# Optimization experiments

Hardware: AMD Instinct MI355X
Metric: run time of the kernel (lower is better)

## Reference

```python
import jax, jax.numpy as jnp
import numpy as np

D_MODEL = 1024
NUM_HEADS = 16
HEAD_DIM = D_MODEL // NUM_HEADS
MAX_SEQ_LEN = 2048
THETA = 10000.0
B, T = 2, 2048


def precompute_cos_sin(head_dim, max_len, theta):
    freqs = 1.0 / theta ** (jnp.arange(0, head_dim, 2, dtype=jnp.float32) / head_dim)
    t = jnp.arange(max_len, dtype=jnp.float32)
    f = jnp.outer(t, freqs)  # [max_len, head_dim//2]
    return jnp.concatenate([jnp.cos(f), jnp.sin(f)], axis=-1)  # [max_len, head_dim]


def apply_rotary_emb(x, cos_sin):
    # x: [B, H, T, Hs]; cos_sin: [T, Hs]
    xr = x.reshape(*x.shape[:-1], -1, 2)
    x1, x2 = xr[..., 0], xr[..., 1]
    cos, sin = jnp.split(cos_sin, 2, axis=-1)  # each [T, Hs//2]
    out = jnp.stack([x1 * cos - x2 * sin, x1 * sin + x2 * cos], axis=-1)
    return out.reshape(x.shape).astype(x.dtype)


def setup_inputs() -> dict:
    key = jax.random.key(0)
    ks = jax.random.split(key, 5)
    scale = 1.0 / np.sqrt(D_MODEL)
    return {
        'x': jax.random.normal(ks[0], (B, T, D_MODEL), dtype=jnp.float32),
        'wq': jax.random.normal(ks[1], (D_MODEL, D_MODEL), dtype=jnp.float32) * scale,
        'wk': jax.random.normal(ks[2], (D_MODEL, D_MODEL), dtype=jnp.float32) * scale,
        'wv': jax.random.normal(ks[3], (D_MODEL, D_MODEL), dtype=jnp.float32) * scale,
        'wo': jax.random.normal(ks[4], (D_MODEL, D_MODEL), dtype=jnp.float32) * scale,
    }


def reference(x, wq, wk, wv, wo):
    seq_len = x.shape[1]
    # Linear: einsum('...i,oi->...o'), weight stored as [out, in]
    q = jnp.einsum('bti,oi->bto', x, wq)
    k = jnp.einsum('bti,oi->bto', x, wk)
    v = jnp.einsum('bti,oi->bto', x, wv)
    # split heads: B T (nH Hs) -> B nH T Hs
    def split_heads(t):
        return t.reshape(t.shape[0], t.shape[1], NUM_HEADS, HEAD_DIM).transpose(0, 2, 1, 3)
    xq, xk, xv = split_heads(q), split_heads(k), split_heads(v)
    cos_sin = precompute_cos_sin(HEAD_DIM, MAX_SEQ_LEN, THETA)[:seq_len]
    xq = apply_rotary_emb(xq, cos_sin)
    xk = apply_rotary_emb(xk, cos_sin)
    scores = jnp.einsum('bhqd,bhkd->bhqk', xq, xk) / jnp.sqrt(jnp.float32(HEAD_DIM))
    causal = jnp.tril(jnp.ones((seq_len, seq_len), dtype=bool))
    scores = jnp.where(causal[None, None], scores, -jnp.inf)
    attn = jax.nn.softmax(scores, axis=-1)
    xo = jnp.einsum('bhqk,bhkd->bhqd', attn, xv)
    xo = xo.transpose(0, 2, 1, 3).reshape(x.shape[0], seq_len, D_MODEL)
    return jnp.einsum('bti,oi->bto', xo, wo)
```

## Files before the change

kernel.cpp:

```cpp
#include <hip/hip_runtime.h>
#include <hip/hip_bf16.h>

typedef __hip_bfloat16 bf16;
using s8v = __attribute__((ext_vector_type(8))) short;
using s4v = __attribute__((ext_vector_type(4))) short;
using f4v = __attribute__((ext_vector_type(4))) float;

#define D_MODEL 1024
#define NHEADS  16
#define HDIM    64
#define TSEQ    2048
#define NBATCH  2
#define BT      (NBATCH * TSEQ)

#define QSCALE  0.180336880111f
#define SBIAS  -17.3123404907f

__device__ inline short f2bf_bits(float f) {
    bf16 h = __float2bfloat16(f);
    return *reinterpret_cast<short*>(&h);
}

__device__ inline void load8(const bf16* p, s8v& o) { o = *(const s8v*)p; }
__device__ inline void load8(const float* p, s8v& o) {
    const f4v a = *(const f4v*)p;
    const f4v b = *(const f4v*)(p + 4);
    s8v r;
    r[0] = f2bf_bits(a[0]); r[1] = f2bf_bits(a[1]);
    r[2] = f2bf_bits(a[2]); r[3] = f2bf_bits(a[3]);
    r[4] = f2bf_bits(b[0]); r[5] = f2bf_bits(b[1]);
    r[6] = f2bf_bits(b[2]); r[7] = f2bf_bits(b[3]);
    o = r;
}

__device__ inline void storeC(bf16* p, float v)  { *p = __float2bfloat16(v); }
__device__ inline void storeC(float* p, float v) { *p = v; }

__device__ inline void gload_lds16(const bf16* g, short* l) {
    __builtin_amdgcn_global_load_lds(
        (__attribute__((address_space(1))) void*)(unsigned long long)(size_t)g,
        (__attribute__((address_space(3))) void*)l,
        16, 0, 0);
}

__device__ inline void stage8(const bf16* g, short* l) { gload_lds16(g, l); }
__device__ inline void stage8(const float* g, short* l) {
    s8v v; load8(g, v); *(s8v*)l = v;
}

__global__ __launch_bounds__(256) void cvt_kernel(
    const float* __restrict__ src, bf16* __restrict__ dst)
{
    const size_t i = ((size_t)blockIdx.x * 256 + threadIdx.x) * 8;
    s8v v; load8(src + i, v);
    *(s8v*)&dst[i] = v;
}

__global__ __launch_bounds__(256) void cvt_all_kernel(
    const float* __restrict__ x,  bf16* __restrict__ xb,
    const float* __restrict__ wq, bf16* __restrict__ wqb,
    const float* __restrict__ wk, bf16* __restrict__ wkb,
    const float* __restrict__ wv, bf16* __restrict__ wvb,
    const float* __restrict__ wo, bf16* __restrict__ wob,
    float2* __restrict__ cs_table)
{
    const int blk = blockIdx.x;
    if (blk >= 4096) {
        const int idx = (blk - 4096) * 256 + threadIdx.x;
        const int tt = idx >> 5;
        const int i  = idx & 31;
        const float inv_freq = expf(-(float)i * (9.210340371976184f / 32.0f));
        float s, c;
        sincosf((float)tt * inv_freq, &s, &c);
        cs_table[idx] = make_float2(c, s);
        return;
    }
    const float* src; bf16* dst; int base;
    if (blk < 2048)      { src = x;  dst = xb;  base = 0; }
    else if (blk < 2560) { src = wq; dst = wqb; base = 2048; }
    else if (blk < 3072) { src = wk; dst = wkb; base = 2560; }
    else if (blk < 3584) { src = wv; dst = wvb; base = 3072; }
    else                 { src = wo; dst = wob; base = 3584; }
    const size_t i = ((size_t)(blk - base) * 256 + threadIdx.x) * 8;
    s8v v; load8(src + i, v);
    *(s8v*)&dst[i] = v;
}

template <int TM, bool ROPE, typename TA, typename TW, typename TC>
__global__ __launch_bounds__(256, 2) void gemm_bt(
    const TA* __restrict__ A,
    const TW* __restrict__ W0, const TW* __restrict__ W1, const TW* __restrict__ W2,
    TC* __restrict__ C0, TC* __restrict__ C1, TC* __restrict__ C2,
    bf16* __restrict__ VT, const float2* __restrict__ cs_table)
{
    const TW* W = (blockIdx.z == 0) ? W0 : (blockIdx.z == 1) ? W1 : W2;
    TC*       C = (blockIdx.z == 0) ? C0 : (blockIdx.z == 1) ? C1 : C2;
    const bool vt_mode = (VT != nullptr) && (blockIdx.z == 2);

    constexpr int K = 1024, N = 1024;
    constexpr int MT = TM / 32;
    __shared__ __align__(16) short As[TM * 64];
    __shared__ __align__(16) short Ws[128 * 64];

    const int t    = threadIdx.x;
    const int lane = t & 63;
    const int wave = t >> 6;
    const int m16  = lane & 15;
    const int quad = lane >> 4;
    const int wm   = (wave >> 1) * (TM / 2);
    const int wn   = (wave & 1) * 64;
    const int rowBase = blockIdx.x * TM;
    const int colBase = blockIdx.y * 128;

    f4v acc[MT][4];
#pragma unroll
    for (int i = 0; i < MT; ++i)
#pragma unroll
        for (int j = 0; j < 4; ++j) acc[i][j] = f4v{0.f, 0.f, 0.f, 0.f};

    for (int kk = 0; kk < K / 64; ++kk) {
#pragma unroll
        for (int r = 0; r < TM / 32; ++r) {
            const int chunk = r * 256 + t;
            const int row   = chunk >> 3;
            const int c8s   = (chunk & 7) ^ (row & 7);
            stage8(A + (size_t)(rowBase + row) * K + kk * 64 + c8s * 8, &As[chunk * 8]);
        }
#pragma unroll
        for (int r = 0; r < 4; ++r) {
            const int chunk = r * 256 + t;
            const int row   = chunk >> 3;
            const int c8s   = (chunk & 7) ^ (row & 7);
            stage8(W + (size_t)(colBase + row) * K + kk * 64 + c8s * 8, &Ws[chunk * 8]);
        }
        __syncthreads();

#pragma unroll
        for (int ks = 0; ks < 2; ++ks) {
            s8v af[MT], bw[4];
#pragma unroll
            for (int mt = 0; mt < MT; ++mt) {
                const int rowa = wm + mt * 16 + m16;
                af[mt] = *(const s8v*)&As[rowa * 64 + ((ks * 4 + quad) ^ (rowa & 7)) * 8];
            }
#pragma unroll
            for (int nt = 0; nt < 4; ++nt) {
                const int roww = wn + nt * 16 + m16;
                bw[nt] = *(const s8v*)&Ws[roww * 64 + ((ks * 4 + quad) ^ (roww & 7)) * 8];
            }
#pragma unroll
            for (int mt = 0; mt < MT; ++mt)
#pragma unroll
                for (int nt = 0; nt < 4; ++nt)
                    acc[mt][nt] = __builtin_amdgcn_mfma_f32_16x16x32_bf16(
                        af[mt], bw[nt], acc[mt][nt], 0, 0, 0);
        }
        __syncthreads();
    }

    if (vt_mode) {
#pragma unroll
        for (int mt = 0; mt < MT; ++mt)
#pragma unroll
            for (int nt = 0; nt < 4; ++nt) {
                const int col  = colBase + wn + nt * 16 + m16;
                const int row0 = rowBase + wm + mt * 16 + quad * 4;
                const int bb   = row0 >> 11;
                const int tt   = row0 & (TSEQ - 1);
                s4v pk;
#pragma unroll
                for (int r = 0; r < 4; ++r) pk[r] = f2bf_bits(acc[mt][nt][r]);
                *(s4v*)&VT[((size_t)(bb * 1024 + col)) * TSEQ + tt] = pk;
            }
    } else {
        const float qs = (ROPE && blockIdx.z == 0) ? QSCALE : 1.0f;
#pragma unroll
        for (int mt = 0; mt < MT; ++mt)
#pragma unroll
            for (int nt = 0; nt < 4; ++nt) {
                const int col = colBase + wn + nt * 16 + m16;
#pragma unroll
                for (int r = 0; r < 4; ++r) {
                    const int row = rowBase + wm + mt * 16 + quad * 4 + r;
                    float v = acc[mt][nt][r];
                    if (ROPE) {
                        const float prt = __shfl_xor(v, 1, 64);
                        const int   tt  = row & (TSEQ - 1);
                        const int   i   = (col & 63) >> 1;
                        const float2 cs = cs_table[tt * 32 + i];
                        v = (col & 1) ? (prt * cs.y + v * cs.x)
                                      : (v * cs.x - prt * cs.y);
                        v *= qs;
                    }
                    storeC(&C[(size_t)row * N + col], v);
                }
            }
    }
}

__global__ __launch_bounds__(256) void rope_inplace(
    bf16* __restrict__ qp, bf16* __restrict__ kp)
{
    const int idx = blockIdx.x * 256 + threadIdx.x;
    const int i  = idx & 31;
    const int h  = (idx >> 5) & (NHEADS - 1);
    const int tt = (idx >> 9) & (TSEQ - 1);
    const int b  = idx >> 20;

    const size_t src = (size_t)(b * TSEQ + tt) * D_MODEL + h * HDIM + 2 * i;

    const float inv_freq = expf(-(float)i * (9.210340371976184f / 32.0f));
    const float f = (float)tt * inv_freq;
    float s, c;
    sincosf(f, &s, &c);

    const float q1 = __bfloat162float(qp[src]);
    const float q2 = __bfloat162float(qp[src + 1]);
    qp[src]     = __float2bfloat16((q1 * c - q2 * s) * QSCALE);
    qp[src + 1] = __float2bfloat16((q1 * s + q2 * c) * QSCALE);

    const float k1 = __bfloat162float(kp[src]);
    const float k2 = __bfloat162float(kp[src + 1]);
    kp[src]     = __float2bfloat16(k1 * c - k2 * s);
    kp[src + 1] = __float2bfloat16(k1 * s + k2 * c);
}

__global__ __launch_bounds__(256, 2) void attn_kernel(
    bf16* __restrict__ qp, const bf16* __restrict__ kp,
    const bf16* __restrict__ vt)
{
    const int hb = blockIdx.x & 31;
    const int ib = blockIdx.x >> 5;
    const int h  = hb & (NHEADS - 1);
    const int b  = hb >> 4;
    const int t    = threadIdx.x;
    const int lane = t & 63;
    const int wave = t >> 6;
    const int m16  = lane & 15;
    const int quad = lane >> 4;

    bf16*       Qb  = qp + (size_t)b * TSEQ * D_MODEL + h * HDIM;
    const bf16* Kb  = kp + (size_t)b * TSEQ * D_MODEL + h * HDIM;
    const bf16* Vtb = vt + ((size_t)b * 1024 + h * HDIM) * TSEQ;

    __shared__ __align__(16) short Klds[128 * 64];
    __shared__ __align__(16) short Vlds[64 * 128];
    __shared__ __align__(16) short P_lds[4][16][136];

    s8v ones;
#pragma unroll
    for (int j = 0; j < 8; ++j) ones[j] = (short)0x3F80;

#pragma unroll 1
    for (int pass = 0; pass < 2; ++pass) {
        const int bx = pass ? (31 - ib) : ib;
        const int q0 = bx * 64 + wave * 16;

        const s8v aq0 = *(const s8v*)&Qb[(size_t)(q0 + m16) * D_MODEL + quad * 8];
        const s8v aq1 = *(const s8v*)&Qb[(size_t)(q0 + m16) * D_MODEL + 32 + quad * 8];

        f4v o_acc[4];
#pragma unroll
        for (int nd = 0; nd < 4; ++nd) o_acc[nd] = f4v{0.f, 0.f, 0.f, 0.f};
        f4v o_l = f4v{0.f, 0.f, 0.f, 0.f};

        const int iters = (bx + 2) >> 1;
#pragma unroll 1
        for (int it = 0; it < iters; ++it) {
            const int kv0 = it * 128;

            __syncthreads();

#pragma unroll
            for (int r = 0; r < 4; ++r) {
                const int chunk = r * 256 + t;
                const int row   = chunk >> 3;
                const int c8s   = (chunk & 7) ^ (row & 7);
                gload_lds16(Kb + (size_t)(kv0 + row) * D_MODEL + c8s * 8,
                            &Klds[chunk * 8]);
            }
#pragma unroll
            for (int r = 0; r < 4; ++r) {
                const int chunk = r * 256 + t;
                const int row   = chunk >> 4;
                const int c16s  = (chunk & 15) ^ (row & 15);
                gload_lds16(Vtb + (size_t)row * TSEQ + kv0 + c16s * 8,
                            &Vlds[chunk * 8]);
            }
            __syncthreads();

            f4v s_acc[8];
#pragma unroll
            for (int nk = 0; nk < 8; ++nk)
                s_acc[nk] = f4v{SBIAS, SBIAS, SBIAS, SBIAS};
#pragma unroll
            for (int nk = 0; nk < 8; ++nk) {
                const int rowk = nk * 16 + m16;
                const int sw   = m16 & 7;
                const s8v bk0 = *(const s8v*)&Klds[rowk * 64 + (quad ^ sw) * 8];
                const s8v bk1 = *(const s8v*)&Klds[rowk * 64 + ((4 + quad) ^ sw) * 8];
                s_acc[nk] = __builtin_amdgcn_mfma_f32_16x16x32_bf16(aq0, bk0, s_acc[nk], 0, 0, 0);
                s_acc[nk] = __builtin_amdgcn_mfma_f32_16x16x32_bf16(aq1, bk1, s_acc[nk], 0, 0, 0);
            }

            const bool diag = (it == iters - 1);
#pragma unroll
            for (int nk = 0; nk < 8; ++nk) {
                const int kv = kv0 + nk * 16 + m16;
#pragma unroll
                for (int r = 0; r < 4; ++r) {
                    float p = __builtin_amdgcn_exp2f(s_acc[nk][r]);
                    if (diag) {
                        const int qi = q0 + quad * 4 + r;
                        p = (kv <= qi) ? p : 0.0f;
                    }
                    P_lds[wave][quad * 4 + r][nk * 16 + m16] = f2bf_bits(p);
                }
            }
            asm volatile("s_waitcnt lgkmcnt(0)" ::: "memory");

#pragma unroll
            for (int kt = 0; kt < 4; ++kt) {
                const s8v ap = *(const s8v*)&P_lds[wave][m16][kt * 32 + quad * 8];
#pragma unroll
                for (int nd = 0; nd < 4; ++nd) {
                    const int rowv = nd * 16 + m16;
                    const s8v bv = *(const s8v*)&Vlds[rowv * 128
                                                      + ((kt * 4 + quad) ^ m16) * 8];
                    o_acc[nd] = __builtin_amdgcn_mfma_f32_16x16x32_bf16(
                        ap, bv, o_acc[nd], 0, 0, 0);
                }
                o_l = __builtin_amdgcn_mfma_f32_16x16x32_bf16(ap, ones, o_l, 0, 0, 0);
            }
        }

        float inv_l[4];
#pragma unroll
        for (int r = 0; r < 4; ++r) inv_l[r] = 1.0f / o_l[r];
#pragma unroll
        for (int nd = 0; nd < 4; ++nd)
#pragma unroll
            for (int r = 0; r < 4; ++r) {
                const int qi = q0 + quad * 4 + r;
                Qb[(size_t)qi * D_MODEL + nd * 16 + m16] =
                    __float2bfloat16(o_acc[nd][r] * inv_l[r]);
            }
    }
}

extern "C" void kernel_launch(void* const* d_in, const int* in_sizes, int n_in,
                              void* d_out, int out_size, void* d_ws, size_t ws_size,
                              hipStream_t stream) {
    const float* x  = (const float*)d_in[0];
    const float* wq = (const float*)d_in[1];
    const float* wk = (const float*)d_in[2];
    const float* wv = (const float*)d_in[3];
    const float* wo = (const float*)d_in[4];
    float* out = (float*)d_out;

    bf16* ws = (bf16*)d_ws;
    const size_t SZ  = (size_t)BT * D_MODEL;
    const size_t SZW = (size_t)D_MODEL * D_MODEL;
    bf16* qp  = ws + 0 * SZ;
    bf16* kp  = ws + 1 * SZ;
    bf16* vt  = (bf16*)d_out;
    bf16* xb  = (bf16*)(out + 2 * 1024 * 1024);

    const size_t need_w    = (2 * SZ + 4 * SZW) * sizeof(bf16);
    const size_t need_full = need_w + 65536 * sizeof(float2);

    if (ws_size >= need_full) {
        bf16*   wqb = ws + 2 * SZ + 0 * SZW;
        bf16*   wkb = ws + 2 * SZ + 1 * SZW;
        bf16*   wvb = ws + 2 * SZ + 2 * SZW;
        bf16*   wob = ws + 2 * SZ + 3 * SZW;
        float2* cst = (float2*)(ws + 2 * SZ + 4 * SZW);

        cvt_all_kernel<<<dim3(4352), 256, 0, stream>>>(
            x, xb, wq, wqb, wk, wkb, wv, wvb, wo, wob, cst);
        gemm_bt<128, true, bf16, bf16, bf16><<<dim3(32, 8, 3), 256, 0, stream>>>(
            xb, wqb, wkb, wvb, qp, kp, qp , vt, cst);
        attn_kernel<<<dim3(512), 256, 0, stream>>>(qp, kp, vt);
        gemm_bt<64, false, bf16, bf16, float><<<dim3(64, 8, 1), 256, 0, stream>>>(
            qp, wob, wob, wob, out, out, out, nullptr, nullptr);
    } else if (ws_size >= need_w) {
        bf16* wqb = ws + 2 * SZ + 0 * SZW;
        bf16* wkb = ws + 2 * SZ + 1 * SZW;
        bf16* wvb = ws + 2 * SZ + 2 * SZW;
        bf16* wob = ws + 2 * SZ + 3 * SZW;
        cvt_all_kernel<<<dim3(4096), 256, 0, stream>>>(
            x, xb, wq, wqb, wk, wkb, wv, wvb, wo, wob, nullptr);
        gemm_bt<128, false, bf16, bf16, bf16><<<dim3(32, 8, 3), 256, 0, stream>>>(
            xb, wqb, wkb, wvb, qp, kp, qp , vt, nullptr);
        rope_inplace<<<dim3(8192), 256, 0, stream>>>(qp, kp);
        attn_kernel<<<dim3(512), 256, 0, stream>>>(qp, kp, vt);
        gemm_bt<64, false, bf16, bf16, float><<<dim3(64, 8, 1), 256, 0, stream>>>(
            qp, wob, wob, wob, out, out, out, nullptr, nullptr);
    } else {
        bf16* wob = kp;
        cvt_kernel<<<dim3(2048), 256, 0, stream>>>(x, xb);
        gemm_bt<128, false, bf16, float, bf16><<<dim3(32, 8, 3), 256, 0, stream>>>(
            xb, wq, wk, wv, qp, kp, qp , vt, nullptr);
        rope_inplace<<<dim3(8192), 256, 0, stream>>>(qp, kp);
        attn_kernel<<<dim3(512), 256, 0, stream>>>(qp, kp, vt);
        cvt_kernel<<<dim3(512), 256, 0, stream>>>(wo, wob);
        gemm_bt<64, false, bf16, bf16, float><<<dim3(64, 8, 1), 256, 0, stream>>>(
            qp, wob, wob, wob, out, out, out, nullptr, nullptr);
    }
}
```

Before: 169.2 us.

## Double-buffer K/V tiles in attention with prefetch, swizzled P LDS, setprio

K and V tiles are now double-buffered in LDS. The next tile's global-to-LDS loads are issued before the current tile is computed, and partial vmcnt waits let those loads overlap the MFMA work. The P scratch buffer is reorganized with an XOR swizzle to reduce LDS bank conflicts in place of the old padded row layout. MFMA regions are wrapped in s_setprio. The change doubles K/V LDS usage to about 80KB per block, which may limit occupancy at the declared 2 blocks per CU, and it relies on manual waitcnt counts being correct.

```diff
diff --git a/kernel.cpp b/kernel.cpp
--- a/kernel.cpp
+++ b/kernel.cpp
@@ -243,13 +243,32 @@
     const bf16* Kb  = kp + (size_t)b * TSEQ * D_MODEL + h * HDIM;
     const bf16* Vtb = vt + ((size_t)b * 1024 + h * HDIM) * TSEQ;
 
-    __shared__ __align__(16) short Klds[128 * 64];
-    __shared__ __align__(16) short Vlds[64 * 128];
-    __shared__ __align__(16) short P_lds[4][16][136];
+    __shared__ __align__(16) short Klds[2][128 * 64];
+    __shared__ __align__(16) short Vlds[2][64 * 128];
+    __shared__ __align__(16) short P_lds[4][16 * 128];
 
     s8v ones;
 #pragma unroll
     for (int j = 0; j < 8; ++j) ones[j] = (short)0x3F80;
+
+    auto stage_kv = [&](int buf, int kv0) {
+#pragma unroll
+        for (int r = 0; r < 4; ++r) {
+            const int chunk = r * 256 + t;
+            const int row   = chunk >> 3;
+            const int c8s   = (chunk & 7) ^ (row & 7);
+            gload_lds16(Kb + (size_t)(kv0 + row) * D_MODEL + c8s * 8,
+                        &Klds[buf][chunk * 8]);
+        }
+#pragma unroll
+        for (int r = 0; r < 4; ++r) {
+            const int chunk = r * 256 + t;
+            const int row   = chunk >> 4;
+            const int c16s  = (chunk & 15) ^ (row & 15);
+            gload_lds16(Vtb + (size_t)row * TSEQ + kv0 + c16s * 8,
+                        &Vlds[buf][chunk * 8]);
+        }
+    };
 
 #pragma unroll 1
     for (int pass = 0; pass < 2; ++pass) {
@@ -265,43 +284,38 @@
         f4v o_l = f4v{0.f, 0.f, 0.f, 0.f};
 
         const int iters = (bx + 2) >> 1;
+
+        stage_kv(0, 0);
+
 #pragma unroll 1
         for (int it = 0; it < iters; ++it) {
+            const int cur = it & 1;
             const int kv0 = it * 128;
 
-            __syncthreads();
-
-#pragma unroll
-            for (int r = 0; r < 4; ++r) {
-                const int chunk = r * 256 + t;
-                const int row   = chunk >> 3;
-                const int c8s   = (chunk & 7) ^ (row & 7);
-                gload_lds16(Kb + (size_t)(kv0 + row) * D_MODEL + c8s * 8,
-                            &Klds[chunk * 8]);
-            }
-#pragma unroll
-            for (int r = 0; r < 4; ++r) {
-                const int chunk = r * 256 + t;
-                const int row   = chunk >> 4;
-                const int c16s  = (chunk & 15) ^ (row & 15);
-                gload_lds16(Vtb + (size_t)row * TSEQ + kv0 + c16s * 8,
-                            &Vlds[chunk * 8]);
-            }
-            __syncthreads();
+            if (it + 1 < iters) {
+                stage_kv(cur ^ 1, kv0 + 128);
+                asm volatile("s_waitcnt vmcnt(8)" ::: "memory");
+            } else {
+                asm volatile("s_waitcnt vmcnt(0)" ::: "memory");
+            }
+            __builtin_amdgcn_s_barrier();
+            __builtin_amdgcn_sched_barrier(0);
 
             f4v s_acc[8];
 #pragma unroll
             for (int nk = 0; nk < 8; ++nk)
                 s_acc[nk] = f4v{SBIAS, SBIAS, SBIAS, SBIAS};
+            __builtin_amdgcn_s_setprio(1);
 #pragma unroll
             for (int nk = 0; nk < 8; ++nk) {
                 const int rowk = nk * 16 + m16;
                 const int sw   = m16 & 7;
-                const s8v bk0 = *(const s8v*)&Klds[rowk * 64 + (quad ^ sw) * 8];
-                const s8v bk1 = *(const s8v*)&Klds[rowk * 64 + ((4 + quad) ^ sw) * 8];
+                const s8v bk0 = *(const s8v*)&Klds[cur][rowk * 64 + (quad ^ sw) * 8];
+                const s8v bk1 = *(const s8v*)&Klds[cur][rowk * 64 + ((4 + quad) ^ sw) * 8];
                 s_acc[nk] = __builtin_amdgcn_mfma_f32_16x16x32_bf16(aq0, bk0, s_acc[nk], 0, 0, 0);
                 s_acc[nk] = __builtin_amdgcn_mfma_f32_16x16x32_bf16(aq1, bk1, s_acc[nk], 0, 0, 0);
             }
+            __builtin_amdgcn_s_setprio(0);
 
             const bool diag = (it == iters - 1);
 #pragma unroll
@@ -314,24 +328,32 @@
                         const int qi = q0 + quad * 4 + r;
                         p = (kv <= qi) ? p : 0.0f;
                     }
-                    P_lds[wave][quad * 4 + r][nk * 16 + m16] = f2bf_bits(p);
+                    const int prow = quad * 4 + r;
+                    const int pchk = (nk * 2 + (m16 >> 3)) ^ (prow & 7);
+                    P_lds[wave][prow * 128 + (pchk << 3) + (m16 & 7)] = f2bf_bits(p);
                 }
             }
             asm volatile("s_waitcnt lgkmcnt(0)" ::: "memory");
 
+            __builtin_amdgcn_s_setprio(1);
 #pragma unroll
             for (int kt = 0; kt < 4; ++kt) {
-                const s8v ap = *(const s8v*)&P_lds[wave][m16][kt * 32 + quad * 8];
+                const int achk = (kt * 4 + quad) ^ (m16 & 7);
+                const s8v ap = *(const s8v*)&P_lds[wave][m16 * 128 + (achk << 3)];
 #pragma unroll
                 for (int nd = 0; nd < 4; ++nd) {
                     const int rowv = nd * 16 + m16;
-                    const s8v bv = *(const s8v*)&Vlds[rowv * 128
+                    const s8v bv = *(const s8v*)&Vlds[cur][rowv * 128
                                                       + ((kt * 4 + quad) ^ m16) * 8];
                     o_acc[nd] = __builtin_amdgcn_mfma_f32_16x16x32_bf16(
                         ap, bv, o_acc[nd], 0, 0, 0);
                 }
                 o_l = __builtin_amdgcn_mfma_f32_16x16x32_bf16(ap, ones, o_l, 0, 0, 0);
             }
+            __builtin_amdgcn_s_setprio(0);
+
+            asm volatile("s_waitcnt lgkmcnt(0)" ::: "memory");
+            __builtin_amdgcn_s_barrier();
         }
 
         float inv_l[4];
```

New measurement: 166.4 us. About the same (-1.6%).
